# Optimization experiments

Measured on AMD Instinct MI355X. Metric: run time of the kernel, lower is better.

Reference implementation:

```python
import jax, jax.numpy as jnp
import numpy as np

N, D_IN, HID, NH = 16384, 2048, 2048, 16
HD = HID // NH  # head_size = 128


def setup_inputs() -> dict:
    key = jax.random.key(0)
    ks = jax.random.split(key, 8)
    s = 1.0 / np.sqrt(D_IN)
    return {
        "protein": jax.random.normal(ks[0], (N, D_IN), jnp.float32),
        "drug": jax.random.normal(ks[1], (N, D_IN), jnp.float32),
        "mask_prot": jnp.ones((N,), bool),
        "mask_drug": jnp.ones((N,), bool),
        "Wq_p": jax.random.uniform(ks[2], (D_IN, HID), jnp.float32, -s, s),
        "Wk_p": jax.random.uniform(ks[3], (D_IN, HID), jnp.float32, -s, s),
        "Wv_p": jax.random.uniform(ks[4], (D_IN, HID), jnp.float32, -s, s),
        "Wq_d": jax.random.uniform(ks[5], (D_IN, HID), jnp.float32, -s, s),
        "Wk_d": jax.random.uniform(ks[6], (D_IN, HID), jnp.float32, -s, s),
        "Wv_d": jax.random.uniform(ks[7], (D_IN, HID), jnp.float32, -s, s),
    }


def _heads(x):
    # [N, L, HID] -> [N, L, NH, HD]
    return x.reshape(x.shape[0], x.shape[1], NH, HD)


def _alpha_logits(logits, mask_row, mask_col, inf=1e6):
    # logits: [N, L1, L2, H]; masks: [N, L1], [N, L2] (broadcast over heads)
    mask_pair = mask_row[:, :, None, None] & mask_col[:, None, :, None]
    logits = jnp.where(mask_pair, logits, logits - inf)
    alpha = jax.nn.softmax(logits, axis=2)
    alpha = jnp.where(mask_row[:, :, None, None], alpha, jnp.zeros_like(alpha))
    return alpha


def reference(protein, drug, mask_prot, mask_drug, Wq_p, Wk_p, Wv_p, Wq_d, Wk_d, Wv_d):
    p = protein[:, None, :]  # [N, 1, D_IN]
    d = drug[:, None, :]
    # forward() overwrites the masks with all-ones of shape [N, L=1]
    m_p = jnp.ones(p.shape[:-1], bool)
    m_d = jnp.ones(d.shape[:-1], bool)

    qp = _heads(jnp.einsum('bld,dh->blh', p, Wq_p))  # [N,1,NH,HD]
    kp = _heads(jnp.einsum('bld,dh->blh', p, Wk_p))
    vp = _heads(jnp.einsum('bld,dh->blh', p, Wv_p))
    qd = _heads(jnp.einsum('bld,dh->blh', d, Wq_d))
    kd = _heads(jnp.einsum('bld,dh->blh', d, Wk_d))
    vd = _heads(jnp.einsum('bld,dh->blh', d, Wv_d))

    logits_pp = jnp.einsum('blhd,bkhd->blkh', qp, kp)
    logits_pd = jnp.einsum('blhd,bkhd->blkh', qp, kd)
    logits_dp = jnp.einsum('blhd,bkhd->blkh', qd, kp)
    logits_dd = jnp.einsum('blhd,bkhd->blkh', qd, kd)

    a_pp = _alpha_logits(logits_pp, m_p, m_p)
    a_pd = _alpha_logits(logits_pd, m_p, m_d)
    a_dp = _alpha_logits(logits_dp, m_d, m_p)
    a_dd = _alpha_logits(logits_dd, m_d, m_d)

    def agg(alpha, v):
        out = jnp.einsum('blkh,bkhd->blhd', alpha, v)
        return out.reshape(out.shape[0], out.shape[1], HID)

    prot_embedding = (agg(a_pp, vp) + agg(a_pd, vd)) / 2  # [N,1,HID]
    drug_embedding = (agg(a_dp, vp) + agg(a_dd, vd)) / 2

    # agg_mode == 'cls'
    prot_embed = prot_embedding[:, 0]
    drug_embed = drug_embedding[:, 0]
    return jnp.concatenate([prot_embed, drug_embed], axis=1)  # [N, 2*HID]
```

## Files before the change

### kernel.cpp

```cpp
#include <hip/hip_runtime.h>
#include <stdint.h>


typedef __attribute__((ext_vector_type(8))) short short8;
typedef __attribute__((ext_vector_type(4))) float float4v;
typedef __attribute__((ext_vector_type(2))) unsigned int uint2v;

typedef const __attribute__((address_space(1))) unsigned int* gp_t;
typedef __attribute__((address_space(3))) unsigned int* lp_t;

#define M_DIM 16384
#define N_DIM 2048
#define K_DIM 4096
#define OUT_LD 4096

static __device__ __forceinline__ unsigned int pack_bf16x2(float x, float y) {
  union { float f; unsigned int u; } a, b;
  a.f = x; b.f = y;
  unsigned int ua = a.u + 0x8000u;
  unsigned int ub = b.u + 0x8000u;
  return __builtin_amdgcn_perm(ub, ua, 0x07060302u);
}

static __device__ __forceinline__ unsigned short f2bf(float x) {
  union { float f; unsigned int u; } a; a.f = x;
  return (unsigned short)((a.u + 0x8000u) >> 16);
}

__global__ __launch_bounds__(256)
void prep_wt(const float* __restrict__ Wp, const float* __restrict__ Wd,
             unsigned short* __restrict__ Wt) {
  __shared__ float tile[32][33];
  const int k0 = blockIdx.x * 32;
  const int n0 = blockIdx.y * 32;
  const int tx = threadIdx.x;
  const int ty = threadIdx.y;
  const float* W = (k0 < 2048) ? Wp : Wd;
  const int kk0 = (k0 < 2048) ? k0 : k0 - 2048;
#pragma unroll
  for (int i = 0; i < 4; ++i) {
    int r = ty * 4 + i;
    tile[r][tx] = W[(size_t)(kk0 + r) * 2048 + n0 + tx];
  }
  __syncthreads();
#pragma unroll
  for (int i = 0; i < 4; ++i) {
    int r = ty * 4 + i;
    Wt[(size_t)(n0 + r) * (size_t)K_DIM + k0 + tx] = f2bf(tile[tx][r]);
  }
}

__global__ __launch_bounds__(256)
void cast_a(const float* __restrict__ P, const float* __restrict__ Dg,
            unsigned int* __restrict__ Abf) {
  int idx = blockIdx.x * 256 + threadIdx.x;
  int row = idx >> 10;
  int j = (idx & 1023) << 2;
  const float* src = (j < 2048) ? (P + (size_t)row * 2048 + j)
                                : (Dg + (size_t)row * 2048 + (j - 2048));
  float4v v = *(const float4v*)src;
  uint2v o;
  o.x = pack_bf16x2(v.x, v.y);
  o.y = pack_bf16x2(v.z, v.w);
  *(uint2v*)(Abf + (size_t)row * 2048 + (j >> 1)) = o;
}


#define VMW(N) asm volatile("s_waitcnt vmcnt(" #N ")" ::: "memory")
#define LGW0() asm volatile("s_waitcnt lgkmcnt(0)" ::: "memory")
#define BAR() __builtin_amdgcn_s_barrier()

#define LOAD_A(Ac, QM)                                                      \
  _Pragma("unroll") for (int i = 0; i < 4; ++i) {                           \
    af[i][0] = *(const short8*)&(Ac)[aoff + ((QM)*4 + i) * 1024 + c0];      \
    af[i][1] = *(const short8*)&(Ac)[aoff + ((QM)*4 + i) * 1024 + c1];      \
  }

#define LOAD_B(Bc, QN)                                                      \
  _Pragma("unroll") for (int j = 0; j < 2; ++j) {                           \
    bfr[j][0] = *(const short8*)&(Bc)[boff + ((QN)*2 + j) * 1024 + c0];     \
    bfr[j][1] = *(const short8*)&(Bc)[boff + ((QN)*2 + j) * 1024 + c1];     \
  }

#define MFMA8(QM, QN)                                                       \
  _Pragma("unroll") for (int i = 0; i < 4; ++i)                             \
  _Pragma("unroll") for (int j = 0; j < 2; ++j) {                           \
    acc[(QM)*4 + i][(QN)*2 + j] = __builtin_amdgcn_mfma_f32_16x16x32_bf16(  \
        af[i][0], bfr[j][0], acc[(QM)*4 + i][(QN)*2 + j], 0, 0, 0);         \
    acc[(QM)*4 + i][(QN)*2 + j] = __builtin_amdgcn_mfma_f32_16x16x32_bf16(  \
        af[i][1], bfr[j][1], acc[(QM)*4 + i][(QN)*2 + j], 0, 0, 0);         \
  }

__global__ __launch_bounds__(512, 2)
void gemm8(const unsigned short* __restrict__ Abf,
           const unsigned short* __restrict__ Wt,
           float* __restrict__ out) {
  __shared__ unsigned short As[2][256 * 64];
  __shared__ unsigned short Bs[2][256 * 64];

  const int t = threadIdx.x;
  const int w = t >> 6, l = t & 63;
  const int wm = w >> 2, wn = w & 3;
  const int lr = l & 15, q16 = l >> 4, xr = lr & 7;

  const int bx = blockIdx.x;
  const int tn = bx & 7, tm = bx >> 3;
  const int m0 = tm << 8, n0 = tn << 8;

  const int srow = t >> 3;
  const int sk = (((t & 7) ^ (srow & 7)) << 3);
  const int brr = srow & 31;
  const int bsel = t >> 8;

  auto stage_a = [&](int buf, int k0, int h) {
#pragma unroll
    for (int sub = 0; sub < 2; ++sub) {
      const int row = m0 + sub * 128 + h * 64 + srow;
      const unsigned short* g = Abf + (size_t)row * K_DIM + (k0 + sk);
      const int ldsrow0 = sub * 128 + h * 64 + (w << 3);
      __builtin_amdgcn_global_load_lds((gp_t)(const void*)g,
                                       (lp_t)&As[buf][ldsrow0 * 64], 16, 0, 0);
    }
  };
  auto stage_b = [&](int buf, int k0, int nh) {
#pragma unroll
    for (int sub = 0; sub < 2; ++sub) {
      const int wnr = sub * 2 + bsel;
      const int ncol = n0 + wnr * 64 + nh * 32 + brr;
      const unsigned short* g = Wt + (size_t)ncol * K_DIM + (k0 + sk);
      const int ldsrow0 = wnr * 64 + nh * 32 + ((w & 3) << 3);
      __builtin_amdgcn_global_load_lds((gp_t)(const void*)g,
                                       (lp_t)&Bs[buf][ldsrow0 * 64], 16, 0, 0);
    }
  };

  float4v acc[8][4];
#pragma unroll
  for (int i = 0; i < 8; ++i)
#pragma unroll
    for (int j = 0; j < 4; ++j)
      acc[i][j] = (float4v){0.f, 0.f, 0.f, 0.f};

  const int aoff = (wm * 128 + lr) * 64;
  const int boff = (wn * 64 + lr) * 64;
  const int c0 = ((q16) ^ xr) << 3;
  const int c1 = ((4 + q16) ^ xr) << 3;

  stage_a(0, 0, 0);
  stage_b(0, 0, 0);
  stage_b(0, 0, 1);
  stage_a(0, 0, 1);
  stage_a(1, 64, 0);
  stage_b(1, 64, 0);
  VMW(8);
  BAR();

  for (int tt = 0; tt < 62; ++tt) {
    const int buf = tt & 1;
    unsigned short* Ac = &As[buf][0];
    unsigned short* Bc = &Bs[buf][0];
    const int k1 = tt * 64 + 64;
    const int k2 = tt * 64 + 128;
    short8 af[4][2];
    short8 bfr[2][2];

    LOAD_A(Ac, 0)
    LOAD_B(Bc, 0)
    stage_b(buf ^ 1, k1, 1);
    VMW(8); BAR(); LGW0();
    __builtin_amdgcn_s_setprio(1);
    MFMA8(0, 0)
    __builtin_amdgcn_s_setprio(0);
    BAR();

    LOAD_B(Bc, 1)
    stage_a(buf ^ 1, k1, 1);
    VMW(8); BAR(); LGW0();
    __builtin_amdgcn_s_setprio(1);
    MFMA8(0, 1)
    __builtin_amdgcn_s_setprio(0);
    BAR();

    LOAD_A(Ac, 1)
    LOAD_B(Bc, 0)
    stage_a(buf, k2, 0);
    VMW(8); BAR(); LGW0();
    __builtin_amdgcn_s_setprio(1);
    MFMA8(1, 0)
    __builtin_amdgcn_s_setprio(0);
    BAR();

    LOAD_B(Bc, 1)
    stage_b(buf, k2, 0);
    VMW(8); BAR(); LGW0();
    __builtin_amdgcn_s_setprio(1);
    MFMA8(1, 1)
    __builtin_amdgcn_s_setprio(0);
    BAR();
  }

  stage_b(1, 4032, 1);
  stage_a(1, 4032, 1);
  VMW(0);
  BAR();
#pragma unroll
  for (int e = 0; e < 2; ++e) {
    unsigned short* Ac = &As[e][0];
    unsigned short* Bc = &Bs[e][0];
    short8 af[4][2];
    short8 bfr[2][2];
    __builtin_amdgcn_s_setprio(1);
    LOAD_A(Ac, 0)
    LOAD_B(Bc, 0)
    MFMA8(0, 0)
    LOAD_B(Bc, 1)
    MFMA8(0, 1)
    LOAD_A(Ac, 1)
    LOAD_B(Bc, 0)
    MFMA8(1, 0)
    LOAD_B(Bc, 1)
    MFMA8(1, 1)
    __builtin_amdgcn_s_setprio(0);
  }

  const int rbase = m0 + wm * 128 + q16 * 4;
  const int cbase = n0 + wn * 64 + lr;
#pragma unroll
  for (int f = 0; f < 8; ++f)
#pragma unroll
    for (int j = 0; j < 4; ++j) {
      const int row = rbase + f * 16;
      const int col = cbase + j * 16;
#pragma unroll
      for (int r = 0; r < 4; ++r) {
        float v = acc[f][j][r] * 0.5f;
        size_t o = (size_t)(row + r) * (size_t)OUT_LD + col;
        out[o] = v;
        out[o + N_DIM] = v;
      }
    }
}

__global__ __launch_bounds__(256)
void gemm_k(const float* __restrict__ Ap, const float* __restrict__ Ad,
            const unsigned short* __restrict__ Wt,
            float* __restrict__ out) {
  __shared__ unsigned short As[128 * 64];
  __shared__ unsigned short Bsm[128 * 64];

  const int t = threadIdx.x;
  const int bx = blockIdx.x;
  const int tn = bx & 15, tm = bx >> 4;
  const int m0 = tm << 7, n0 = tn << 7;
  const int w = t >> 6, l = t & 63;
  const int wmm = w & 1, wnn = w >> 1;
  const int lr = l & 15, q = l >> 4;

  const int rB = t >> 3;
  const int kB = (t & 7) * 8;

  float4v acc[4][4];
#pragma unroll
  for (int i = 0; i < 4; ++i)
#pragma unroll
    for (int j = 0; j < 4; ++j)
      acc[i][j] = (float4v){0.f, 0.f, 0.f, 0.f};

  for (int k0 = 0; k0 < K_DIM; k0 += 64) {
#pragma unroll
    for (int i = 0; i < 4; ++i) {
      const unsigned short* g =
          Wt + (size_t)(n0 + i * 32 + rB) * (size_t)K_DIM + (k0 + kB);
      __builtin_amdgcn_global_load_lds((gp_t)(const void*)g,
                                       (lp_t)&Bsm[i * 2048 + w * 512], 16, 0, 0);
    }
    {
      const float* base;
      int kk;
      if (k0 < 2048) { base = Ap; kk = k0; } else { base = Ad; kk = k0 - 2048; }
      const int rA = t >> 4;
      const int cA = (t & 15) * 4;
#pragma unroll
      for (int i = 0; i < 8; ++i) {
        int m = i * 16 + rA;
        float4v v = *(const float4v*)(base + (size_t)(m0 + m) * 2048 + kk + cA);
        uint2v o;
        o.x = pack_bf16x2(v.x, v.y);
        o.y = pack_bf16x2(v.z, v.w);
        *(uint2v*)&As[m * 64 + cA] = o;
      }
    }
    __syncthreads();

#pragma unroll
    for (int ks = 0; ks < 2; ++ks) {
      short8 a2[4], b2[4];
#pragma unroll
      for (int i = 0; i < 4; ++i) {
        a2[i] = *(const short8*)&As[(wmm * 64 + i * 16 + lr) * 64 + ks * 32 + q * 8];
        b2[i] = *(const short8*)&Bsm[(wnn * 64 + i * 16 + lr) * 64 + ks * 32 + q * 8];
      }
#pragma unroll
      for (int i = 0; i < 4; ++i)
#pragma unroll
        for (int j = 0; j < 4; ++j)
          acc[i][j] = __builtin_amdgcn_mfma_f32_16x16x32_bf16(a2[i], b2[j],
                                                              acc[i][j], 0, 0, 0);
    }
    __syncthreads();
  }

#pragma unroll
  for (int i = 0; i < 4; ++i) {
    const int r0 = m0 + wmm * 64 + i * 16 + q * 4;
#pragma unroll
    for (int j = 0; j < 4; ++j) {
      const int c = n0 + wnn * 64 + j * 16 + lr;
#pragma unroll
      for (int r = 0; r < 4; ++r) {
        float v = acc[i][j][r] * 0.5f;
        size_t o = (size_t)(r0 + r) * (size_t)OUT_LD + c;
        out[o] = v;
        out[o + 2048] = v;
      }
    }
  }
}

__global__ __launch_bounds__(256)
void gemm_fallback(const float* __restrict__ P, const float* __restrict__ Dg,
                   const float* __restrict__ Wp, const float* __restrict__ Wd,
                   float* __restrict__ out) {
  __shared__ float Asf[64][17];
  __shared__ float Bsf[16][65];
  const int bx = blockIdx.x;
  const int by = blockIdx.y;
  const int t = threadIdx.x;
  const int tc = t & 15, trw = t >> 4;
  const int m0 = by * 64, n0 = bx * 64;
  float accf[4][4] = {};
  for (int k0 = 0; k0 < 4096; k0 += 16) {
    const float* Asrc = (k0 < 2048) ? P : Dg;
    const float* Bsrc = (k0 < 2048) ? Wp : Wd;
    const int kk = k0 & 2047;
#pragma unroll
    for (int i = 0; i < 4; ++i) {
      int r = i * 16 + trw;
      Asf[r][tc] = Asrc[(size_t)(m0 + r) * 2048 + kk + tc];
    }
#pragma unroll
    for (int i = 0; i < 4; ++i) {
      int r = i * 4 + (t >> 6);
      int c = t & 63;
      Bsf[r][c] = Bsrc[(size_t)(kk + r) * 2048 + n0 + c];
    }
    __syncthreads();
#pragma unroll
    for (int k2 = 0; k2 < 16; ++k2) {
      float a[4], b[4];
#pragma unroll
      for (int i = 0; i < 4; ++i) a[i] = Asf[trw * 4 + i][k2];
#pragma unroll
      for (int j = 0; j < 4; ++j) b[j] = Bsf[k2][tc * 4 + j];
#pragma unroll
      for (int i = 0; i < 4; ++i)
#pragma unroll
        for (int j = 0; j < 4; ++j) accf[i][j] += a[i] * b[j];
    }
    __syncthreads();
  }
#pragma unroll
  for (int i = 0; i < 4; ++i)
#pragma unroll
    for (int j = 0; j < 4; ++j) {
      float v = accf[i][j] * 0.5f;
      size_t o = (size_t)(m0 + trw * 4 + i) * 4096 + n0 + tc * 4 + j;
      out[o] = v;
      out[o + 2048] = v;
    }
}

extern "C" void kernel_launch(void* const* d_in, const int* in_sizes, int n_in,
                              void* d_out, int out_size, void* d_ws, size_t ws_size,
                              hipStream_t stream) {
  const float* protein = (const float*)d_in[0];
  const float* drug    = (const float*)d_in[1];
  const float* Wv_p    = (const float*)d_in[6];
  const float* Wv_d    = (const float*)d_in[9];
  float* out = (float*)d_out;

  const size_t wt_bytes = (size_t)N_DIM * K_DIM * sizeof(unsigned short);
  const size_t a_bytes  = (size_t)M_DIM * K_DIM * sizeof(unsigned short);

  if (ws_size >= wt_bytes) {
    unsigned short* Wt = (unsigned short*)d_ws;
    prep_wt<<<dim3(128, 64), dim3(32, 8), 0, stream>>>(Wv_p, Wv_d, Wt);
    if (ws_size >= wt_bytes + a_bytes) {
      unsigned int* Abf = (unsigned int*)((char*)d_ws + wt_bytes);
      cast_a<<<65536, 256, 0, stream>>>(protein, drug, Abf);
      gemm8<<<512, 512, 0, stream>>>((const unsigned short*)Abf, Wt, out);
    } else {
      gemm_k<<<2048, 256, 0, stream>>>(protein, drug, Wt, out);
    }
  } else {
    gemm_fallback<<<dim3(32, 256), 256, 0, stream>>>(protein, drug, Wv_p, Wv_d, out);
  }
}
```

Before: 807.5 us.

## Restructure GEMM pipeline: keep both B fragments in registers, serpentine order, remap blocks

Keeps both B fragment sets in registers so the (1,1)/(1,0) quadrants reuse them in serpentine order instead of reloading from LDS. Moves all staging of the next tile into the current buffer after its fragments are read, with a single vmcnt wait per iteration. Also remaps block index so consecutive blocks share the same N tile column rather than the same M row, changing cache reuse. The extra fragment registers raise VGPR pressure and the staging-into-current-buffer timing must be race-free.

```diff
diff --git a/kernel.cpp b/kernel.cpp
--- a/kernel.cpp
+++ b/kernel.cpp
@@ -76,19 +76,19 @@
     af[i][1] = *(const short8*)&(Ac)[aoff + ((QM)*4 + i) * 1024 + c1];      \
   }
 
-#define LOAD_B(Bc, QN)                                                      \
+#define LOAD_B2(dst, Bc, QN)                                                \
   _Pragma("unroll") for (int j = 0; j < 2; ++j) {                           \
-    bfr[j][0] = *(const short8*)&(Bc)[boff + ((QN)*2 + j) * 1024 + c0];     \
-    bfr[j][1] = *(const short8*)&(Bc)[boff + ((QN)*2 + j) * 1024 + c1];     \
-  }
-
-#define MFMA8(QM, QN)                                                       \
+    dst[j][0] = *(const short8*)&(Bc)[boff + ((QN)*2 + j) * 1024 + c0];     \
+    dst[j][1] = *(const short8*)&(Bc)[boff + ((QN)*2 + j) * 1024 + c1];     \
+  }
+
+#define MFMA_Q(bset, QM, QN)                                                \
   _Pragma("unroll") for (int i = 0; i < 4; ++i)                             \
   _Pragma("unroll") for (int j = 0; j < 2; ++j) {                           \
     acc[(QM)*4 + i][(QN)*2 + j] = __builtin_amdgcn_mfma_f32_16x16x32_bf16(  \
-        af[i][0], bfr[j][0], acc[(QM)*4 + i][(QN)*2 + j], 0, 0, 0);         \
+        af[i][0], bset[j][0], acc[(QM)*4 + i][(QN)*2 + j], 0, 0, 0);        \
     acc[(QM)*4 + i][(QN)*2 + j] = __builtin_amdgcn_mfma_f32_16x16x32_bf16(  \
-        af[i][1], bfr[j][1], acc[(QM)*4 + i][(QN)*2 + j], 0, 0, 0);         \
+        af[i][1], bset[j][1], acc[(QM)*4 + i][(QN)*2 + j], 0, 0, 0);        \
   }
 
 __global__ __launch_bounds__(512, 2)
@@ -104,7 +104,8 @@
   const int lr = l & 15, q16 = l >> 4, xr = lr & 7;
 
   const int bx = blockIdx.x;
-  const int tn = bx & 7, tm = bx >> 3;
+  const int logical = (bx & 7) * 64 + (bx >> 3);
+  const int tn = logical & 7, tm = logical >> 3;
   const int m0 = tm << 8, n0 = tn << 8;
 
   const int srow = t >> 3;
@@ -143,7 +144,7 @@
 
   const int aoff = (wm * 128 + lr) * 64;
   const int boff = (wn * 64 + lr) * 64;
-  const int c0 = ((q16) ^ xr) << 3;
+  const int c0 = (q16 ^ xr) << 3;
   const int c1 = ((4 + q16) ^ xr) << 3;
 
   stage_a(0, 0, 0);
@@ -152,6 +153,8 @@
   stage_a(0, 0, 1);
   stage_a(1, 64, 0);
   stage_b(1, 64, 0);
+  stage_b(1, 64, 1);
+  stage_a(1, 64, 1);
   VMW(8);
   BAR();
 
@@ -159,48 +162,45 @@
     const int buf = tt & 1;
     unsigned short* Ac = &As[buf][0];
     unsigned short* Bc = &Bs[buf][0];
-    const int k1 = tt * 64 + 64;
     const int k2 = tt * 64 + 128;
     short8 af[4][2];
-    short8 bfr[2][2];
+    short8 b0r[2][2];
+    short8 b1r[2][2];
 
     LOAD_A(Ac, 0)
-    LOAD_B(Bc, 0)
-    stage_b(buf ^ 1, k1, 1);
-    VMW(8); BAR(); LGW0();
+    LOAD_B2(b0r, Bc, 0)
+    BAR(); LGW0();
     __builtin_amdgcn_s_setprio(1);
-    MFMA8(0, 0)
+    MFMA_Q(b0r, 0, 0)
     __builtin_amdgcn_s_setprio(0);
     BAR();
 
-    LOAD_B(Bc, 1)
-    stage_a(buf ^ 1, k1, 1);
-    VMW(8); BAR(); LGW0();
+    LOAD_B2(b1r, Bc, 1)
+    stage_a(buf, k2, 0);
+    stage_b(buf, k2, 0);
+    BAR(); LGW0();
     __builtin_amdgcn_s_setprio(1);
-    MFMA8(0, 1)
+    MFMA_Q(b1r, 0, 1)
     __builtin_amdgcn_s_setprio(0);
     BAR();
 
     LOAD_A(Ac, 1)
-    LOAD_B(Bc, 0)
-    stage_a(buf, k2, 0);
-    VMW(8); BAR(); LGW0();
+    stage_b(buf, k2, 1);
+    BAR(); LGW0();
     __builtin_amdgcn_s_setprio(1);
-    MFMA8(1, 0)
+    MFMA_Q(b1r, 1, 1)
     __builtin_amdgcn_s_setprio(0);
     BAR();
 
-    LOAD_B(Bc, 1)
-    stage_b(buf, k2, 0);
-    VMW(8); BAR(); LGW0();
+    stage_a(buf, k2, 1);
+    BAR();
     __builtin_amdgcn_s_setprio(1);
-    MFMA8(1, 1)
+    MFMA_Q(b0r, 1, 0)
     __builtin_amdgcn_s_setprio(0);
+    VMW(8);
     BAR();
   }
 
-  stage_b(1, 4032, 1);
-  stage_a(1, 4032, 1);
   VMW(0);
   BAR();
 #pragma unroll
@@ -208,18 +208,17 @@
     unsigned short* Ac = &As[e][0];
     unsigned short* Bc = &Bs[e][0];
     short8 af[4][2];
-    short8 bfr[2][2];
+    short8 b0r[2][2];
+    short8 b1r[2][2];
     __builtin_amdgcn_s_setprio(1);
     LOAD_A(Ac, 0)
-    LOAD_B(Bc, 0)
-    MFMA8(0, 0)
-    LOAD_B(Bc, 1)
-    MFMA8(0, 1)
+    LOAD_B2(b0r, Bc, 0)
+    MFMA_Q(b0r, 0, 0)
+    LOAD_B2(b1r, Bc, 1)
+    MFMA_Q(b1r, 0, 1)
     LOAD_A(Ac, 1)
-    LOAD_B(Bc, 0)
-    MFMA8(1, 0)
-    LOAD_B(Bc, 1)
-    MFMA8(1, 1)
+    MFMA_Q(b1r, 1, 1)
+    MFMA_Q(b0r, 1, 0)
     __builtin_amdgcn_s_setprio(0);
   }
 
```

Measured after the change: 825.8 us. +2.3%, slower.
